# Kernel tuning notes

Hardware: AMD Instinct MI355X
Metric: run time of the kernel (lower is better)

The kernel has to match this reference:

```python
import jax, jax.numpy as jnp
import numpy as np

B, S, HID = 2, 1024, 4096
NH, NKV, HD = 32, 8, 128
GROUPS = NH // NKV  # 4
BITS = 8
SCALING = HD ** -0.5


def quantize_lastdim(x, bits=BITS):
    """Asymmetric min-max fake-quant per row of the last dim (groupsize=-1),
    matching ActQuantizer.find_params + quantize/dequantize."""
    qmax = float(2 ** bits - 1)
    xmin = jnp.minimum(jnp.min(x, axis=-1, keepdims=True), 0.0)
    xmax = jnp.maximum(jnp.max(x, axis=-1, keepdims=True), 0.0)
    rng = xmax - xmin
    scale = jnp.where(rng == 0, 1.0, rng / qmax)
    zero = jnp.round(-xmin / scale)
    q = jnp.clip(jnp.round(x / scale) + zero, 0.0, qmax)
    return (q - zero) * scale


def rotate_half(x):
    x1, x2 = jnp.split(x, 2, axis=-1)
    return jnp.concatenate([-x2, x1], axis=-1)


def setup_inputs() -> dict:
    key = jax.random.key(0)
    ks = jax.random.split(key, 5)
    hidden_states = jax.random.normal(ks[0], (B, S, HID), dtype=jnp.float32)
    w_std = 0.02
    Wq = w_std * jax.random.normal(ks[1], (NH * HD, HID), dtype=jnp.float32)
    Wk = w_std * jax.random.normal(ks[2], (NKV * HD, HID), dtype=jnp.float32)
    Wv = w_std * jax.random.normal(ks[3], (NKV * HD, HID), dtype=jnp.float32)
    Wo = w_std * jax.random.normal(ks[4], (HID, NH * HD), dtype=jnp.float32)
    # RoPE tables (theta=10000)
    inv_freq = 1.0 / (10000.0 ** (jnp.arange(0, HD, 2, dtype=jnp.float32) / HD))
    freqs = jnp.outer(jnp.arange(S, dtype=jnp.float32), inv_freq)  # [S, HD/2]
    emb = jnp.concatenate([freqs, freqs], axis=-1)  # [S, HD]
    cos = jnp.broadcast_to(jnp.cos(emb)[None], (B, S, HD)).astype(jnp.float32)
    sin = jnp.broadcast_to(jnp.sin(emb)[None], (B, S, HD)).astype(jnp.float32)
    # additive causal mask [B,1,S,S]
    causal = jnp.tril(jnp.ones((S, S), dtype=bool))
    attention_mask = jnp.where(causal, 0.0, -1e9).astype(jnp.float32)
    attention_mask = jnp.broadcast_to(attention_mask[None, None], (B, 1, S, S))
    return {"hidden_states": hidden_states, "cos": cos, "sin": sin,
            "attention_mask": attention_mask, "Wq": Wq, "Wk": Wk, "Wv": Wv, "Wo": Wo}


def reference(hidden_states, cos, sin, attention_mask, Wq, Wk, Wv, Wo):
    b, s, _ = hidden_states.shape
    # projections -> [B, H, S, D]
    q = (hidden_states @ Wq.T).reshape(b, s, NH, HD).transpose(0, 2, 1, 3)
    k = (hidden_states @ Wk.T).reshape(b, s, NKV, HD).transpose(0, 2, 1, 3)
    v = (hidden_states @ Wv.T).reshape(b, s, NKV, HD).transpose(0, 2, 1, 3)
    # RoPE (HF: unsqueeze cos/sin at head dim)
    c = cos[:, None, :, :]
    si = sin[:, None, :, :]
    q = q * c + rotate_half(q) * si
    k = k * c + rotate_half(k) * si
    # SmoothK per-channel: subtract per-channel mean over the sequence
    # (softmax-invariant outlier smoothing of K before quantization)
    k = k - jnp.mean(k, axis=2, keepdims=True)
    # activation fake-quant of Q, K (per token over head_dim)
    q = quantize_lastdim(q)
    k = quantize_lastdim(k)
    # V quantized along the sequence axis (module transposes dims 2,3 first)
    v = quantize_lastdim(v.transpose(0, 1, 3, 2)).transpose(0, 1, 3, 2)
    # GQA repeat
    k_rep = jnp.repeat(k, GROUPS, axis=1)
    v_rep = jnp.repeat(v, GROUPS, axis=1)
    scores = jnp.einsum('bhqd,bhkd->bhqk', q, k_rep) * SCALING + attention_mask
    w = jax.nn.softmax(scores.astype(jnp.float32), axis=-1).astype(q.dtype)
    # fake-quant attention weights per row (groupsize=-1, so no padding)
    w = quantize_lastdim(w)
    attn = jnp.einsum('bhqk,bhkd->bhqd', w, v_rep)
    attn = attn.transpose(0, 2, 1, 3).reshape(b, s, NH * HD)
    out = attn @ Wo.T
    return (out, w)
```

## Files before the change

kernel.cpp:

```cpp
#include <hip/hip_runtime.h>
#include <math.h>
#include <stdint.h>

typedef unsigned int u32;
typedef unsigned short u16;
typedef __bf16 bf16x8 __attribute__((ext_vector_type(8)));
typedef float f32x4 __attribute__((ext_vector_type(4)));
typedef unsigned short u16x8 __attribute__((ext_vector_type(8)));
typedef unsigned short u16x4 __attribute__((ext_vector_type(4)));

constexpr int   Bb  = 2;
constexpr int   Ss  = 1024;
constexpr int   HID = 4096;
constexpr int   NH  = 32;
constexpr int   NKV = 8;
constexpr int   HD  = 128;
constexpr float SCALING = 0.0883883476483184405501f;

enum { M_QKV = 0, M_OUT = 3 };

__device__ __forceinline__ u16 f2bf(float f) {
  u32 u = __builtin_bit_cast(u32, f);
  u = u + 0x7fffu + ((u >> 16) & 1u);
  return (u16)(u >> 16);
}

__device__ __forceinline__ void gld_lds16(const void* g, void* l) {
  __builtin_amdgcn_global_load_lds(
      (const __attribute__((address_space(1))) u32*)(uintptr_t)g,
      (__attribute__((address_space(3))) u32*)(uintptr_t)l, 16, 0, 0);
}

template <int MODE>
__global__ __launch_bounds__(256, 2) void mfma_gemm(
    const u16* __restrict__ Abf_g,
    const u16* __restrict__ B0, const u16* __restrict__ B1,
    const u16* __restrict__ B2,
    float* __restrict__ Cf, float* __restrict__ Ck, float* __restrict__ Cv,
    int K) {
  __shared__ u16 As[3][128 * 32];
  __shared__ u16 Bs[3][256 * 32];

  const int tid = threadIdx.x;
  const int lane = tid & 63;
  const int wid = tid >> 6;
  const int wr = wid >> 1;
  const int wc = wid & 1;
  const int fr = lane & 15;
  const int fq = lane >> 4;

  const int bx = blockIdx.x;
  const int m0 = blockIdx.y * 128;
  int nloc = 0;

  const u16* Abf = Abf_g + (size_t)m0 * K;
  const u16* Bp = nullptr;
  int which = 0;

  if (MODE == M_QKV) {
    if (bx < 16)      { which = 0; Bp = B0 + (size_t)bx * 256 * K;        nloc = bx * 256; }
    else if (bx < 20) { which = 1; Bp = B1 + (size_t)(bx - 16) * 256 * K; nloc = (bx - 16) * 256; }
    else              { which = 2; Bp = B2 + (size_t)(bx - 20) * 256 * K; nloc = (bx - 20) * 256; }
  } else {
    Bp = B0 + (size_t)bx * 256 * K;
    nloc = bx * 256;
  }

  f32x4 acc[4][8];
#pragma unroll
  for (int i = 0; i < 4; i++)
#pragma unroll
    for (int j = 0; j < 8; j++) acc[i][j] = (f32x4){0.f, 0.f, 0.f, 0.f};

  const int prow = wid * 16 + (lane >> 2);
  const int psl = lane & 3;

  auto stA = [&](int t, int s, int e) {
    const int row = e * 64 + prow;
    gld_lds16(Abf + (size_t)row * K + t * 32 + ((psl ^ ((row >> 1) & 3)) * 8),
              &As[s][(e * 64 + wid * 16) * 32]);
  };
  auto stB = [&](int t, int s, int e) {
    const int row = e * 64 + prow;
    gld_lds16(Bp + (size_t)row * K + t * 32 + ((psl ^ ((row >> 1) & 3)) * 8),
              &Bs[s][(e * 64 + wid * 16) * 32]);
  };

  const int nk = K >> 5;

  stA(0, 0, 0); stA(0, 0, 1);
  stB(0, 0, 0); stB(0, 0, 1); stB(0, 0, 2); stB(0, 0, 3);
  stA(1, 1, 0); stA(1, 1, 1);
  stB(1, 1, 0); stB(1, 1, 1); stB(1, 1, 2); stB(1, 1, 3);
  asm volatile("s_waitcnt vmcnt(6)" ::: "memory");
  __builtin_amdgcn_sched_barrier(0);
  __builtin_amdgcn_s_barrier();

  int buf = 0, nxt = 2;
  for (int kt = 0; kt < nk; ++kt) {
    const bool st = (kt + 2 < nk);
    bf16x8 av[4], bv[4];

#pragma unroll
    for (int i = 0; i < 4; ++i) {
      const int r = wr * 64 + i * 16 + fr;
      av[i] = *(const bf16x8*)&As[buf][r * 32 + ((fq ^ ((r >> 1) & 3)) * 8)];
    }
#pragma unroll
    for (int j = 0; j < 4; ++j) {
      const int r = wc * 128 + j * 16 + fr;
      bv[j] = *(const bf16x8*)&Bs[buf][r * 32 + ((fq ^ ((r >> 1) & 3)) * 8)];
    }
    if (st) { stA(kt + 2, nxt, 0); stA(kt + 2, nxt, 1); stB(kt + 2, nxt, 0); }
    __builtin_amdgcn_s_barrier();
    asm volatile("s_waitcnt lgkmcnt(0)" ::: "memory");
    __builtin_amdgcn_sched_barrier(0);
    __builtin_amdgcn_s_setprio(1);
#pragma unroll
    for (int i = 0; i < 4; i++)
#pragma unroll
      for (int j = 0; j < 4; j++)
        acc[i][j] = __builtin_amdgcn_mfma_f32_16x16x32_bf16(av[i], bv[j], acc[i][j], 0, 0, 0);
    __builtin_amdgcn_s_setprio(0);

#pragma unroll
    for (int j = 0; j < 4; ++j) {
      const int r = wc * 128 + (j + 4) * 16 + fr;
      bv[j] = *(const bf16x8*)&Bs[buf][r * 32 + ((fq ^ ((r >> 1) & 3)) * 8)];
    }
    if (st) { stB(kt + 2, nxt, 1); stB(kt + 2, nxt, 2); stB(kt + 2, nxt, 3); }
    __builtin_amdgcn_s_barrier();
    asm volatile("s_waitcnt lgkmcnt(0)" ::: "memory");
    __builtin_amdgcn_sched_barrier(0);
    __builtin_amdgcn_s_setprio(1);
#pragma unroll
    for (int i = 0; i < 4; i++)
#pragma unroll
      for (int j = 0; j < 4; j++)
        acc[i][j + 4] = __builtin_amdgcn_mfma_f32_16x16x32_bf16(av[i], bv[j], acc[i][j + 4], 0, 0, 0);
    __builtin_amdgcn_s_setprio(0);

    if (st) {
      asm volatile("s_waitcnt vmcnt(6)" ::: "memory");
    } else {
      asm volatile("s_waitcnt vmcnt(0)" ::: "memory");
    }
    __builtin_amdgcn_sched_barrier(0);
    __builtin_amdgcn_s_barrier();
    buf = (buf == 2) ? 0 : buf + 1;
    nxt = (nxt == 2) ? 0 : nxt + 1;
  }

#pragma unroll
  for (int i = 0; i < 4; i++) {
#pragma unroll
    for (int j = 0; j < 8; j++) {
      const int n = nloc + wc * 128 + j * 16 + fr;
      const int mb = m0 + wr * 64 + i * 16 + fq * 4;
      if (MODE == M_QKV && which == 2) {
        const int b = mb >> 10, s = mb & 1023, h = n >> 7, d = n & 127;
        float4 v4 = {acc[i][j][0], acc[i][j][1], acc[i][j][2], acc[i][j][3]};
        *(float4*)&Cv[((size_t)(b * NKV + h) * HD + d) * Ss + s] = v4;
      } else {
#pragma unroll
        for (int e = 0; e < 4; e++) {
          const int m = mb + e;
          float val = acc[i][j][e];
          if (MODE == M_QKV) {
            const int b = m >> 10, s = m & 1023, h = n >> 7, d = n & 127;
            if (which == 0) Cf[((size_t)(b * NH + h) * Ss + s) * HD + d] = val;
            else            Ck[((size_t)(b * NKV + h) * Ss + s) * HD + d] = val;
          } else {
            Cf[(size_t)m * HID + n] = val;
          }
        }
      }
    }
  }
}

__global__ __launch_bounds__(256) void fused_attn(
    const u16* __restrict__ qb,
    const u16* __restrict__ kb,
    const u16* __restrict__ vTb,
    float* __restrict__ wout,
    u16* __restrict__ attnb) {
  __shared__ u16 Ks[2][64 * 128];
  __shared__ u16 Vs[2][128 * 64];
  __shared__ u16 plds[4][16 * 64];
  __shared__ float scl_l[4][16];

  const int a = 15 - (int)(blockIdx.x >> 6);
  const int bh = blockIdx.x & 63;
  const int b = bh >> 5, h = bh & 31;
  const int kv = h >> 2;
  const int tid = threadIdx.x;
  const int lane = tid & 63;
  const int wq = tid >> 6;
  const int fr = lane & 15, fq = lane >> 4;

  const int nt = a + 1;
  const int Q0 = a * 64;
  const int qw0 = Q0 + wq * 16;

  const u16* Kb = kb + (size_t)(b * NKV + kv) * Ss * HD;
  const u16* Vb = vTb + (size_t)(b * NKV + kv) * HD * Ss;
  float* wrow = wout + (size_t)bh * Ss * Ss;

  auto stageK = [&](int t, int s) {
#pragma unroll
    for (int c = 0; c < 4; ++c) {
      const int idx0 = (c * 4 + wq) * 64;
      const int idx = idx0 + lane;
      const int row = idx >> 4, sl = idx & 15;
      const int slot = sl ^ (row & 15);
      gld_lds16(Kb + (size_t)(t * 64 + row) * HD + slot * 8, &Ks[s][idx0 * 8]);
    }
  };
  auto stageV = [&](int t, int s) {
#pragma unroll
    for (int c = 0; c < 4; ++c) {
      const int idx0 = (c * 4 + wq) * 64;
      const int idx = idx0 + lane;
      const int d = idx >> 3, sl = idx & 7;
      const int slot = sl ^ (d & 7);
      gld_lds16(Vb + (size_t)d * Ss + t * 64 + slot * 8, &Vs[s][idx0 * 8]);
    }
  };

  stageK(0, 0);

  if (a < 15) {
    const int base = 64 * nt;
    const int n4 = 16 * (15 - a);
#pragma unroll
    for (int r0 = 0; r0 < 4; ++r0) {
      const int row = Q0 + r0 * 16 + (tid >> 4);
      float4* wp = (float4*)&wrow[(size_t)row * Ss + base];
      for (int c = tid & 15; c < n4; c += 16) wp[c] = float4{0.f, 0.f, 0.f, 0.f};
    }
  }

  bf16x8 qf[4];
#pragma unroll
  for (int kk = 0; kk < 4; kk++)
    qf[kk] = *(const bf16x8*)&qb[((size_t)bh * Ss + qw0 + fr) * HD + kk * 32 + fq * 8];

  float m[4], l[4];
#pragma unroll
  for (int i = 0; i < 4; i++) { m[i] = -1e30f; l[i] = 0.f; }

  for (int t = 0; t < nt; ++t) {
    if (t + 1 < nt) {
      stageK(t + 1, (t + 1) & 1);
      asm volatile("s_waitcnt vmcnt(4)" ::: "memory");
    } else {
      asm volatile("s_waitcnt vmcnt(0)" ::: "memory");
    }
    __builtin_amdgcn_sched_barrier(0);
    __builtin_amdgcn_s_barrier();
    const u16* Kt = &Ks[t & 1][0];

    f32x4 sa[4];
#pragma unroll
    for (int jn = 0; jn < 4; jn++) sa[jn] = (f32x4){0.f, 0.f, 0.f, 0.f};
#pragma unroll
    for (int kk = 0; kk < 4; ++kk) {
      bf16x8 kfv[4];
#pragma unroll
      for (int jn = 0; jn < 4; ++jn) {
        const int row = jn * 16 + fr;
        kfv[jn] = *(const bf16x8*)&Kt[row * 128 + (((kk * 4 + fq) ^ fr) * 8)];
      }
#pragma unroll
      for (int jn = 0; jn < 4; ++jn)
        sa[jn] = __builtin_amdgcn_mfma_f32_16x16x32_bf16(qf[kk], kfv[jn], sa[jn], 0, 0, 0);
    }

    const bool diag = (t == a);
#pragma unroll
    for (int e = 0; e < 4; ++e) {
      const int qrow = qw0 + fq * 4 + e;
      float sv[4];
      float rmax = -1e30f;
#pragma unroll
      for (int jn = 0; jn < 4; ++jn) {
        float s = sa[jn][e] * SCALING;
        if (diag && (t * 64 + jn * 16 + fr > qrow)) s = -1e30f;
        sv[jn] = s;
        rmax = fmaxf(rmax, s);
      }
#pragma unroll
      for (int o = 1; o < 16; o <<= 1) rmax = fmaxf(rmax, __shfl_xor(rmax, o));
      const float mn = fmaxf(m[e], rmax);
      const float cc = __expf(m[e] - mn);
      float rs = __expf(sv[0] - mn) + __expf(sv[1] - mn) +
                 __expf(sv[2] - mn) + __expf(sv[3] - mn);
#pragma unroll
      for (int o = 1; o < 16; o <<= 1) rs += __shfl_xor(rs, o);
      l[e] = l[e] * cc + rs;
      m[e] = mn;
    }
    __builtin_amdgcn_s_barrier();
  }

  float scl[4];
#pragma unroll
  for (int e = 0; e < 4; e++) scl[e] = 1.f / (255.f * l[e]);
  if (fr == 0) {
#pragma unroll
    for (int e = 0; e < 4; e++) scl_l[wq][fq * 4 + e] = scl[e];
  }

  f32x4 acc2[8];
#pragma unroll
  for (int j = 0; j < 8; j++) acc2[j] = (f32x4){0.f, 0.f, 0.f, 0.f};

  u16* pl = &plds[wq][0];
  const int wrrow = lane >> 2, wrq = lane & 3;
  const float sclr = scl_l[wq][wrrow];

  stageK(0, 0);
  stageV(0, 0);
  for (int t = 0; t < nt; ++t) {
    if (t + 1 < nt) {
      stageK(t + 1, (t + 1) & 1);
      stageV(t + 1, (t + 1) & 1);
      asm volatile("s_waitcnt vmcnt(8)" ::: "memory");
    } else {
      asm volatile("s_waitcnt vmcnt(0)" ::: "memory");
    }
    __builtin_amdgcn_sched_barrier(0);
    __builtin_amdgcn_s_barrier();
    const u16* Kt = &Ks[t & 1][0];
    const u16* Vt = &Vs[t & 1][0];

    f32x4 sa[4];
#pragma unroll
    for (int jn = 0; jn < 4; jn++) sa[jn] = (f32x4){0.f, 0.f, 0.f, 0.f};
#pragma unroll
    for (int kk = 0; kk < 4; ++kk) {
      bf16x8 kfv[4];
#pragma unroll
      for (int jn = 0; jn < 4; ++jn) {
        const int row = jn * 16 + fr;
        kfv[jn] = *(const bf16x8*)&Kt[row * 128 + (((kk * 4 + fq) ^ fr) * 8)];
      }
#pragma unroll
      for (int jn = 0; jn < 4; ++jn)
        sa[jn] = __builtin_amdgcn_mfma_f32_16x16x32_bf16(qf[kk], kfv[jn], sa[jn], 0, 0, 0);
    }

    const bool diag = (t == a);
#pragma unroll
    for (int e = 0; e < 4; ++e) {
      const int qrow = qw0 + fq * 4 + e;
      const int r16 = fq * 4 + e;
#pragma unroll
      for (int jn = 0; jn < 4; ++jn) {
        const int kc = t * 64 + jn * 16 + fr;
        float qv = 0.f;
        if (!diag || kc <= qrow)
          qv = rintf(fminf(255.f * __expf(sa[jn][e] * SCALING - m[e]), 255.f));
        const int col = jn * 16 + fr;
        const int byte = r16 * 128 + (((col >> 3) ^ (r16 & 7)) * 16) + (col & 7) * 2;
        *(u16*)((char*)pl + byte) = f2bf(qv);
      }
    }

    {
      const int s0 = (2 * wrq) ^ (wrrow & 7);
      const int s1 = (2 * wrq + 1) ^ (wrrow & 7);
      bf16x8 p0 = *(const bf16x8*)((char*)pl + wrrow * 128 + s0 * 16);
      bf16x8 p1 = *(const bf16x8*)((char*)pl + wrrow * 128 + s1 * 16);
      float* wp = &wrow[(size_t)(qw0 + wrrow) * Ss + t * 64 + wrq * 16];
      float4 o0, o1, o2, o3;
      o0.x = (float)p0[0] * sclr; o0.y = (float)p0[1] * sclr;
      o0.z = (float)p0[2] * sclr; o0.w = (float)p0[3] * sclr;
      o1.x = (float)p0[4] * sclr; o1.y = (float)p0[5] * sclr;
      o1.z = (float)p0[6] * sclr; o1.w = (float)p0[7] * sclr;
      o2.x = (float)p1[0] * sclr; o2.y = (float)p1[1] * sclr;
      o2.z = (float)p1[2] * sclr; o2.w = (float)p1[3] * sclr;
      o3.x = (float)p1[4] * sclr; o3.y = (float)p1[5] * sclr;
      o3.z = (float)p1[6] * sclr; o3.w = (float)p1[7] * sclr;
      ((float4*)wp)[0] = o0; ((float4*)wp)[1] = o1;
      ((float4*)wp)[2] = o2; ((float4*)wp)[3] = o3;
    }

#pragma unroll
    for (int kk2 = 0; kk2 < 2; ++kk2) {
      const bf16x8 pa = *(const bf16x8*)((char*)pl + fr * 128 + (((kk2 * 4 + fq) ^ (fr & 7)) * 16));
#pragma unroll
      for (int jn2 = 0; jn2 < 8; ++jn2) {
        const int d = jn2 * 16 + fr;
        const bf16x8 vb = *(const bf16x8*)&Vt[d * 64 + (((kk2 * 4 + fq) ^ (d & 7)) * 8)];
        acc2[jn2] = __builtin_amdgcn_mfma_f32_16x16x32_bf16(pa, vb, acc2[jn2], 0, 0, 0);
      }
    }
    __builtin_amdgcn_s_barrier();
  }

#pragma unroll
  for (int e = 0; e < 4; ++e) {
    const int qrow = qw0 + fq * 4 + e;
#pragma unroll
    for (int jn2 = 0; jn2 < 8; ++jn2)
      attnb[((size_t)b * Ss + qrow) * HID + h * HD + jn2 * 16 + fr] =
          f2bf(acc2[jn2][e] * scl[e]);
  }
}

constexpr int CB_HS = Bb * Ss * HID / 2048;
constexpr int CB_WQ = NH * HD * HID / 2048;
constexpr int CB_WK = NKV * HD * HID / 2048;
constexpr int CB_WV = CB_WK;
constexpr int CB_WO = HID * NH * HD / 2048;

__global__ __launch_bounds__(256) void convert_all(
    const float* __restrict__ hs, const float* __restrict__ wq,
    const float* __restrict__ wk, const float* __restrict__ wv,
    const float* __restrict__ wo,
    u16* __restrict__ hsb, u16* __restrict__ wqb, u16* __restrict__ wkb,
    u16* __restrict__ wvb, u16* __restrict__ wob) {
  const int bid = blockIdx.x;
  const float* src;
  u16* dst;
  int base;
  if (bid < CB_HS) { src = hs; dst = hsb; base = 0; }
  else if (bid < CB_HS + CB_WQ) { src = wq; dst = wqb; base = CB_HS; }
  else if (bid < CB_HS + CB_WQ + CB_WK) { src = wk; dst = wkb; base = CB_HS + CB_WQ; }
  else if (bid < CB_HS + CB_WQ + CB_WK + CB_WV) { src = wv; dst = wvb; base = CB_HS + CB_WQ + CB_WK; }
  else { src = wo; dst = wob; base = CB_HS + CB_WQ + CB_WK + CB_WV; }
  const int i = (bid - base) * 256 + threadIdx.x;
  float4 a = ((const float4*)src)[2 * i];
  float4 b = ((const float4*)src)[2 * i + 1];
  u16x8 t;
  t[0] = f2bf(a.x); t[1] = f2bf(a.y); t[2] = f2bf(a.z); t[3] = f2bf(a.w);
  t[4] = f2bf(b.x); t[5] = f2bf(b.y); t[6] = f2bf(b.z); t[7] = f2bf(b.w);
  ((u16x8*)dst)[i] = t;
}

constexpr int PQ_Q = (Bb * NH * Ss) / 4;
constexpr int PQ_K = (Bb * NKV * Ss) / 4;
constexpr int PQ_V = Bb * NKV * HD;

__global__ __launch_bounds__(256) void postq(
    const float* __restrict__ q, u16* __restrict__ qb,
    float* __restrict__ k,
    const float* __restrict__ vT, u16* __restrict__ vTb,
    const float* __restrict__ cs, const float* __restrict__ sn) {
  const int bid = blockIdx.x;
  if (bid < PQ_Q) {
    const int row = bid * 4 + (threadIdx.x >> 6);
    const int lane = threadIdx.x & 63;
    const int s = row & (Ss - 1);
    const int b = row >> 15;
    const float* p = q + (size_t)row * HD;
    const float* cp = cs + ((size_t)b * Ss + s) * HD;
    const float* sp = sn + ((size_t)b * Ss + s) * HD;
    float x1 = p[lane], x2 = p[lane + 64];
    float r1 = x1 * cp[lane] - x2 * sp[lane];
    float r2 = x2 * cp[lane + 64] + x1 * sp[lane + 64];
    float mn = fminf(0.f, fminf(r1, r2));
    float mx = fmaxf(0.f, fmaxf(r1, r2));
#pragma unroll
    for (int o = 32; o; o >>= 1) {
      mn = fminf(mn, __shfl_xor(mn, o));
      mx = fmaxf(mx, __shfl_xor(mx, o));
    }
    float rng = mx - mn;
    float scale = (rng == 0.f) ? 1.f : rng / 255.f;
    float zero = rintf(-mn / scale);
    float q1 = fminf(fmaxf(rintf(r1 / scale) + zero, 0.f), 255.f);
    float q2 = fminf(fmaxf(rintf(r2 / scale) + zero, 0.f), 255.f);
    qb[(size_t)row * HD + lane] = f2bf((q1 - zero) * scale);
    qb[(size_t)row * HD + lane + 64] = f2bf((q2 - zero) * scale);
  } else if (bid < PQ_Q + PQ_K) {
    const int row = (bid - PQ_Q) * 4 + (threadIdx.x >> 6);
    const int lane = threadIdx.x & 63;
    const int s = row & (Ss - 1);
    const int b = row >> 13;
    float* p = k + (size_t)row * HD;
    const float* cp = cs + ((size_t)b * Ss + s) * HD;
    const float* sp = sn + ((size_t)b * Ss + s) * HD;
    float x1 = p[lane], x2 = p[lane + 64];
    float r1 = x1 * cp[lane] - x2 * sp[lane];
    float r2 = x2 * cp[lane + 64] + x1 * sp[lane + 64];
    p[lane] = r1;
    p[lane + 64] = r2;
  } else {
    const int vb = bid - PQ_Q - PQ_K;
    const float* p = vT + (size_t)vb * Ss;
    const int t = threadIdx.x;
    float4 x = ((const float4*)p)[t];
    float mn = fminf(0.f, fminf(fminf(x.x, x.y), fminf(x.z, x.w)));
    float mx = fmaxf(0.f, fmaxf(fmaxf(x.x, x.y), fmaxf(x.z, x.w)));
#pragma unroll
    for (int o = 32; o; o >>= 1) {
      mn = fminf(mn, __shfl_xor(mn, o));
      mx = fmaxf(mx, __shfl_xor(mx, o));
    }
    __shared__ float smn[4], smx[4];
    const int wid = t >> 6, lane = t & 63;
    if (lane == 0) { smn[wid] = mn; smx[wid] = mx; }
    __syncthreads();
    mn = fminf(fminf(smn[0], smn[1]), fminf(smn[2], smn[3]));
    mx = fmaxf(fmaxf(smx[0], smx[1]), fmaxf(smx[2], smx[3]));
    float rng = mx - mn;
    float scale = (rng == 0.f) ? 1.f : rng / 255.f;
    float zero = rintf(-mn / scale);
    u16x4 o4;
    o4[0] = f2bf((fminf(fmaxf(rintf(x.x / scale) + zero, 0.f), 255.f) - zero) * scale);
    o4[1] = f2bf((fminf(fmaxf(rintf(x.y / scale) + zero, 0.f), 255.f) - zero) * scale);
    o4[2] = f2bf((fminf(fmaxf(rintf(x.z / scale) + zero, 0.f), 255.f) - zero) * scale);
    o4[3] = f2bf((fminf(fmaxf(rintf(x.w / scale) + zero, 0.f), 255.f) - zero) * scale);
    ((u16x4*)vTb)[(size_t)vb * 256 + t] = o4;
  }
}

__global__ __launch_bounds__(1024) void kmean_kernel(const float* __restrict__ k,
                                                     float* __restrict__ kmean) {
  const int bh = blockIdx.x;
  const int d = threadIdx.x & 127;
  const int sl = threadIdx.x >> 7;
  const float* p = k + (size_t)bh * Ss * HD;
  float sum = 0.f;
  for (int s = sl; s < Ss; s += 8) sum += p[(size_t)s * HD + d];
  __shared__ float lds[8][128];
  lds[sl][d] = sum;
  __syncthreads();
  if (threadIdx.x < 128) {
    float t = 0.f;
#pragma unroll
    for (int i = 0; i < 8; i++) t += lds[i][threadIdx.x];
    kmean[bh * HD + threadIdx.x] = t * (1.f / 1024.f);
  }
}

__global__ __launch_bounds__(256) void k_subquant(const float* __restrict__ k,
                                                  u16* __restrict__ kb,
                                                  const float* __restrict__ kmean) {
  const int row = blockIdx.x * 4 + (threadIdx.x >> 6);
  const int lane = threadIdx.x & 63;
  const int bh = row >> 10;
  const float* p = k + (size_t)row * HD;
  float x1 = p[lane] - kmean[bh * HD + lane];
  float x2 = p[lane + 64] - kmean[bh * HD + lane + 64];
  float mn = fminf(0.f, fminf(x1, x2));
  float mx = fmaxf(0.f, fmaxf(x1, x2));
#pragma unroll
  for (int o = 32; o; o >>= 1) {
    mn = fminf(mn, __shfl_xor(mn, o));
    mx = fmaxf(mx, __shfl_xor(mx, o));
  }
  float rng = mx - mn;
  float scale = (rng == 0.f) ? 1.f : rng / 255.f;
  float zero = rintf(-mn / scale);
  float q1 = fminf(fmaxf(rintf(x1 / scale) + zero, 0.f), 255.f);
  float q2 = fminf(fmaxf(rintf(x2 / scale) + zero, 0.f), 255.f);
  kb[(size_t)row * HD + lane] = f2bf((q1 - zero) * scale);
  kb[(size_t)row * HD + lane + 64] = f2bf((q2 - zero) * scale);
}

extern "C" void kernel_launch(void* const* d_in, const int* in_sizes, int n_in,
                              void* d_out, int out_size, void* d_ws, size_t ws_size,
                              hipStream_t stream) {
  const float* hs = (const float*)d_in[0];
  const float* cosp = (const float*)d_in[1];
  const float* sinp = (const float*)d_in[2];
  const float* Wq = (const float*)d_in[4];
  const float* Wk = (const float*)d_in[5];
  const float* Wv = (const float*)d_in[6];
  const float* Wo = (const float*)d_in[7];

  float* out = (float*)d_out;
  float* wout = out + (size_t)Bb * Ss * HID;

  char* wsp = (char*)d_ws;
  auto alloc = [&](size_t bytes) {
    char* p = wsp;
    wsp += (bytes + 255) & ~(size_t)255;
    return p;
  };
  float* q     = (float*)alloc((size_t)Bb * NH * Ss * HD * 4);
  float* k     = (float*)alloc((size_t)Bb * NKV * Ss * HD * 4);
  float* vT    = (float*)alloc((size_t)Bb * NKV * Ss * HD * 4);
  float* kmean = (float*)alloc((size_t)Bb * NKV * HD * 4);
  u16* hsb = (u16*)alloc((size_t)Bb * Ss * HID * 2);
  u16* qb  = (u16*)alloc((size_t)Bb * NH * Ss * HD * 2);
  u16* kb  = (u16*)alloc((size_t)Bb * NKV * Ss * HD * 2);
  u16* vTb = (u16*)alloc((size_t)Bb * NKV * Ss * HD * 2);
  u16* Wqb = (u16*)alloc((size_t)NH * HD * HID * 2);
  u16* Wkb = (u16*)alloc((size_t)NKV * HD * HID * 2);
  u16* Wvb = (u16*)alloc((size_t)NKV * HD * HID * 2);
  u16* Wob = (u16*)alloc((size_t)HID * NH * HD * 2);
  u16* attnb = (u16*)q;

  convert_all<<<CB_HS + CB_WQ + CB_WK + CB_WV + CB_WO, 256, 0, stream>>>(
      hs, Wq, Wk, Wv, Wo, hsb, Wqb, Wkb, Wvb, Wob);

  mfma_gemm<M_QKV><<<dim3(24, 16), 256, 0, stream>>>(
      hsb, Wqb, Wkb, Wvb, q, k, vT, HID);

  postq<<<PQ_Q + PQ_K + PQ_V, 256, 0, stream>>>(q, qb, k, vT, vTb, cosp, sinp);
  kmean_kernel<<<Bb * NKV, 1024, 0, stream>>>(k, kmean);
  k_subquant<<<(Bb * NKV * Ss) / 4, 256, 0, stream>>>(k, kb, kmean);

  fused_attn<<<dim3(1024), 256, 0, stream>>>(qb, kb, vTb, wout, attnb);

  mfma_gemm<M_OUT><<<dim3(16, 16), 256, 0, stream>>>(
      attnb, Wob, nullptr, nullptr, out, nullptr, nullptr, HID);
}
```

Measured before the change: 430.1 us.

## Fuse RoPE and Q fake-quant into QKV GEMM epilogue

After: 419.7 us. -2.4%, faster.

```diff
diff --git a/kernel.cpp b/kernel.cpp
--- a/kernel.cpp
+++ b/kernel.cpp
@@ -36,7 +36,9 @@
     const u16* __restrict__ Abf_g,
     const u16* __restrict__ B0, const u16* __restrict__ B1,
     const u16* __restrict__ B2,
-    float* __restrict__ Cf, float* __restrict__ Ck, float* __restrict__ Cv,
+    u16* __restrict__ Cq, float* __restrict__ Ckf, float* __restrict__ Cv,
+    float* __restrict__ Cfo,
+    const float* __restrict__ cosp, const float* __restrict__ sinp,
     int K) {
   __shared__ u16 As[3][128 * 32];
   __shared__ u16 Bs[3][256 * 32];
@@ -151,28 +153,66 @@
     nxt = (nxt == 2) ? 0 : nxt + 1;
   }
 
-#pragma unroll
-  for (int i = 0; i < 4; i++) {
-#pragma unroll
-    for (int j = 0; j < 8; j++) {
-      const int n = nloc + wc * 128 + j * 16 + fr;
-      const int mb = m0 + wr * 64 + i * 16 + fq * 4;
-      if (MODE == M_QKV && which == 2) {
-        const int b = mb >> 10, s = mb & 1023, h = n >> 7, d = n & 127;
-        float4 v4 = {acc[i][j][0], acc[i][j][1], acc[i][j][2], acc[i][j][3]};
-        *(float4*)&Cv[((size_t)(b * NKV + h) * HD + d) * Ss + s] = v4;
-      } else {
-#pragma unroll
-        for (int e = 0; e < 4; e++) {
-          const int m = mb + e;
-          float val = acc[i][j][e];
-          if (MODE == M_QKV) {
-            const int b = m >> 10, s = m & 1023, h = n >> 7, d = n & 127;
-            if (which == 0) Cf[((size_t)(b * NH + h) * Ss + s) * HD + d] = val;
-            else            Ck[((size_t)(b * NKV + h) * Ss + s) * HD + d] = val;
-          } else {
-            Cf[(size_t)m * HID + n] = val;
+  if (MODE == M_QKV && which <= 1) {
+#pragma unroll
+    for (int i = 0; i < 4; i++) {
+#pragma unroll
+      for (int e = 0; e < 4; e++) {
+        const int m = m0 + wr * 64 + i * 16 + fq * 4 + e;
+        const int b = m >> 10, s = m & 1023;
+        const float* cp = cosp + ((size_t)b * Ss + s) * HD;
+        const float* sp2 = sinp + ((size_t)b * Ss + s) * HD;
+        float r[8];
+#pragma unroll
+        for (int j = 0; j < 4; j++) {
+          const float c = cp[j * 16 + fr];
+          const float sv = sp2[j * 16 + fr];
+          const float x1 = acc[i][j][e], x2 = acc[i][j + 4][e];
+          r[j] = x1 * c - x2 * sv;
+          r[j + 4] = x2 * c + x1 * sv;
+        }
+        if (which == 0) {
+          float mn = 0.f, mx = 0.f;
+#pragma unroll
+          for (int j = 0; j < 8; j++) { mn = fminf(mn, r[j]); mx = fmaxf(mx, r[j]); }
+#pragma unroll
+          for (int o = 1; o < 16; o <<= 1) {
+            mn = fminf(mn, __shfl_xor(mn, o));
+            mx = fmaxf(mx, __shfl_xor(mx, o));
           }
+          const float rng = mx - mn;
+          const float scale = (rng == 0.f) ? 1.f : rng / 255.f;
+          const float zero = rintf(-mn / scale);
+          const int hq = bx * 2 + wc;
+          u16* qp = Cq + ((size_t)(b * NH + hq) * Ss + s) * HD + fr;
+#pragma unroll
+          for (int j = 0; j < 8; j++) {
+            const float qv = fminf(fmaxf(rintf(r[j] / scale) + zero, 0.f), 255.f);
+            qp[j * 16] = f2bf((qv - zero) * scale);
+          }
+        } else {
+          const int kh = (bx - 16) * 2 + wc;
+          float* kp = Ckf + ((size_t)(b * NKV + kh) * Ss + s) * HD + fr;
+#pragma unroll
+          for (int j = 0; j < 8; j++) kp[j * 16] = r[j];
+        }
+      }
+    }
+  } else {
+#pragma unroll
+    for (int i = 0; i < 4; i++) {
+#pragma unroll
+      for (int j = 0; j < 8; j++) {
+        const int n = nloc + wc * 128 + j * 16 + fr;
+        const int mb = m0 + wr * 64 + i * 16 + fq * 4;
+        if (MODE == M_QKV) {
+          const int b = mb >> 10, s = mb & 1023, h = n >> 7, d = n & 127;
+          float4 v4 = {acc[i][j][0], acc[i][j][1], acc[i][j][2], acc[i][j][3]};
+          *(float4*)&Cv[((size_t)(b * NKV + h) * HD + d) * Ss + s] = v4;
+        } else {
+#pragma unroll
+          for (int e = 0; e < 4; e++)
+            Cfo[(size_t)(mb + e) * HID + n] = acc[i][j][e];
         }
       }
     }
@@ -440,82 +480,33 @@
   ((u16x8*)dst)[i] = t;
 }
 
-constexpr int PQ_Q = (Bb * NH * Ss) / 4;
-constexpr int PQ_K = (Bb * NKV * Ss) / 4;
-constexpr int PQ_V = Bb * NKV * HD;
-
-__global__ __launch_bounds__(256) void postq(
-    const float* __restrict__ q, u16* __restrict__ qb,
-    float* __restrict__ k,
-    const float* __restrict__ vT, u16* __restrict__ vTb,
-    const float* __restrict__ cs, const float* __restrict__ sn) {
-  const int bid = blockIdx.x;
-  if (bid < PQ_Q) {
-    const int row = bid * 4 + (threadIdx.x >> 6);
-    const int lane = threadIdx.x & 63;
-    const int s = row & (Ss - 1);
-    const int b = row >> 15;
-    const float* p = q + (size_t)row * HD;
-    const float* cp = cs + ((size_t)b * Ss + s) * HD;
-    const float* sp = sn + ((size_t)b * Ss + s) * HD;
-    float x1 = p[lane], x2 = p[lane + 64];
-    float r1 = x1 * cp[lane] - x2 * sp[lane];
-    float r2 = x2 * cp[lane + 64] + x1 * sp[lane + 64];
-    float mn = fminf(0.f, fminf(r1, r2));
-    float mx = fmaxf(0.f, fmaxf(r1, r2));
-#pragma unroll
-    for (int o = 32; o; o >>= 1) {
-      mn = fminf(mn, __shfl_xor(mn, o));
-      mx = fmaxf(mx, __shfl_xor(mx, o));
-    }
-    float rng = mx - mn;
-    float scale = (rng == 0.f) ? 1.f : rng / 255.f;
-    float zero = rintf(-mn / scale);
-    float q1 = fminf(fmaxf(rintf(r1 / scale) + zero, 0.f), 255.f);
-    float q2 = fminf(fmaxf(rintf(r2 / scale) + zero, 0.f), 255.f);
-    qb[(size_t)row * HD + lane] = f2bf((q1 - zero) * scale);
-    qb[(size_t)row * HD + lane + 64] = f2bf((q2 - zero) * scale);
-  } else if (bid < PQ_Q + PQ_K) {
-    const int row = (bid - PQ_Q) * 4 + (threadIdx.x >> 6);
-    const int lane = threadIdx.x & 63;
-    const int s = row & (Ss - 1);
-    const int b = row >> 13;
-    float* p = k + (size_t)row * HD;
-    const float* cp = cs + ((size_t)b * Ss + s) * HD;
-    const float* sp = sn + ((size_t)b * Ss + s) * HD;
-    float x1 = p[lane], x2 = p[lane + 64];
-    float r1 = x1 * cp[lane] - x2 * sp[lane];
-    float r2 = x2 * cp[lane + 64] + x1 * sp[lane + 64];
-    p[lane] = r1;
-    p[lane + 64] = r2;
-  } else {
-    const int vb = bid - PQ_Q - PQ_K;
-    const float* p = vT + (size_t)vb * Ss;
-    const int t = threadIdx.x;
-    float4 x = ((const float4*)p)[t];
-    float mn = fminf(0.f, fminf(fminf(x.x, x.y), fminf(x.z, x.w)));
-    float mx = fmaxf(0.f, fmaxf(fmaxf(x.x, x.y), fmaxf(x.z, x.w)));
-#pragma unroll
-    for (int o = 32; o; o >>= 1) {
-      mn = fminf(mn, __shfl_xor(mn, o));
-      mx = fmaxf(mx, __shfl_xor(mx, o));
-    }
-    __shared__ float smn[4], smx[4];
-    const int wid = t >> 6, lane = t & 63;
-    if (lane == 0) { smn[wid] = mn; smx[wid] = mx; }
-    __syncthreads();
-    mn = fminf(fminf(smn[0], smn[1]), fminf(smn[2], smn[3]));
-    mx = fmaxf(fmaxf(smx[0], smx[1]), fmaxf(smx[2], smx[3]));
-    float rng = mx - mn;
-    float scale = (rng == 0.f) ? 1.f : rng / 255.f;
-    float zero = rintf(-mn / scale);
-    u16x4 o4;
-    o4[0] = f2bf((fminf(fmaxf(rintf(x.x / scale) + zero, 0.f), 255.f) - zero) * scale);
-    o4[1] = f2bf((fminf(fmaxf(rintf(x.y / scale) + zero, 0.f), 255.f) - zero) * scale);
-    o4[2] = f2bf((fminf(fmaxf(rintf(x.z / scale) + zero, 0.f), 255.f) - zero) * scale);
-    o4[3] = f2bf((fminf(fmaxf(rintf(x.w / scale) + zero, 0.f), 255.f) - zero) * scale);
-    ((u16x4*)vTb)[(size_t)vb * 256 + t] = o4;
-  }
+__global__ __launch_bounds__(256) void vquant(const float* __restrict__ vT,
+                                              u16* __restrict__ vTb) {
+  const float* p = vT + (size_t)blockIdx.x * Ss;
+  const int t = threadIdx.x;
+  float4 x = ((const float4*)p)[t];
+  float mn = fminf(0.f, fminf(fminf(x.x, x.y), fminf(x.z, x.w)));
+  float mx = fmaxf(0.f, fmaxf(fmaxf(x.x, x.y), fmaxf(x.z, x.w)));
+#pragma unroll
+  for (int o = 32; o; o >>= 1) {
+    mn = fminf(mn, __shfl_xor(mn, o));
+    mx = fmaxf(mx, __shfl_xor(mx, o));
+  }
+  __shared__ float smn[4], smx[4];
+  const int wid = t >> 6, lane = t & 63;
+  if (lane == 0) { smn[wid] = mn; smx[wid] = mx; }
+  __syncthreads();
+  mn = fminf(fminf(smn[0], smn[1]), fminf(smn[2], smn[3]));
+  mx = fmaxf(fmaxf(smx[0], smx[1]), fmaxf(smx[2], smx[3]));
+  float rng = mx - mn;
+  float scale = (rng == 0.f) ? 1.f : rng / 255.f;
+  float zero = rintf(-mn / scale);
+  u16x4 o4;
+  o4[0] = f2bf((fminf(fmaxf(rintf(x.x / scale) + zero, 0.f), 255.f) - zero) * scale);
+  o4[1] = f2bf((fminf(fmaxf(rintf(x.y / scale) + zero, 0.f), 255.f) - zero) * scale);
+  o4[2] = f2bf((fminf(fmaxf(rintf(x.z / scale) + zero, 0.f), 255.f) - zero) * scale);
+  o4[3] = f2bf((fminf(fmaxf(rintf(x.w / scale) + zero, 0.f), 255.f) - zero) * scale);
+  ((u16x4*)vTb)[(size_t)blockIdx.x * 256 + t] = o4;
 }
 
 __global__ __launch_bounds__(1024) void kmean_kernel(const float* __restrict__ k,
@@ -582,7 +573,6 @@
     wsp += (bytes + 255) & ~(size_t)255;
     return p;
   };
-  float* q     = (float*)alloc((size_t)Bb * NH * Ss * HD * 4);
   float* k     = (float*)alloc((size_t)Bb * NKV * Ss * HD * 4);
   float* vT    = (float*)alloc((size_t)Bb * NKV * Ss * HD * 4);
   float* kmean = (float*)alloc((size_t)Bb * NKV * HD * 4);
@@ -594,20 +584,21 @@
   u16* Wkb = (u16*)alloc((size_t)NKV * HD * HID * 2);
   u16* Wvb = (u16*)alloc((size_t)NKV * HD * HID * 2);
   u16* Wob = (u16*)alloc((size_t)HID * NH * HD * 2);
-  u16* attnb = (u16*)q;
+  u16* attnb = (u16*)alloc((size_t)Bb * Ss * HID * 2);
 
   convert_all<<<CB_HS + CB_WQ + CB_WK + CB_WV + CB_WO, 256, 0, stream>>>(
       hs, Wq, Wk, Wv, Wo, hsb, Wqb, Wkb, Wvb, Wob);
 
   mfma_gemm<M_QKV><<<dim3(24, 16), 256, 0, stream>>>(
-      hsb, Wqb, Wkb, Wvb, q, k, vT, HID);
-
-  postq<<<PQ_Q + PQ_K + PQ_V, 256, 0, stream>>>(q, qb, k, vT, vTb, cosp, sinp);
+      hsb, Wqb, Wkb, Wvb, qb, k, vT, nullptr, cosp, sinp, HID);
+
+  vquant<<<Bb * NKV * HD, 256, 0, stream>>>(vT, vTb);
   kmean_kernel<<<Bb * NKV, 1024, 0, stream>>>(k, kmean);
   k_subquant<<<(Bb * NKV * Ss) / 4, 256, 0, stream>>>(k, kb, kmean);
 
   fused_attn<<<dim3(1024), 256, 0, stream>>>(qb, kb, vTb, wout, attnb);
 
   mfma_gemm<M_OUT><<<dim3(16, 16), 256, 0, stream>>>(
-      attnb, Wob, nullptr, nullptr, out, nullptr, nullptr, HID);
-}
+      attnb, Wob, nullptr, nullptr, nullptr, nullptr, nullptr, out,
+      nullptr, nullptr, HID);
+}
```
